# Kernel optimization log

Hardware: AMD Instinct MI355X
Metric: run time of the kernel (lower is better)

Reference implementation:

```python
import jax, jax.numpy as jnp
import numpy as np

TEMPERATURE = 0.8
TOP_K = 50
TOP_P = 0.9
REP_PENALTY = 1.2
FILTER_VALUE = -1e9  # stands in for -inf in HF top_k_top_p_filtering (numerically identical probs)

B, S, V = 16, 64, 50257
P = 64  # previously generated tokens per sequence


def setup_inputs() -> dict:
    key = jax.random.key(0)
    k1, k2 = jax.random.split(key)
    logits = jax.random.normal(k1, (B, S, V), dtype=jnp.float32) * 3.0
    prev_tokens = jax.random.randint(k2, (S, P), 0, V)
    return {"logits": logits, "prev_tokens": prev_tokens}


def _repetition_penalty(logits, prev_tokens):
    # logits: [B,S,V], prev_tokens: [S,P]
    gathered = jnp.take_along_axis(logits, prev_tokens[None, :, :], axis=-1)  # [B,S,P]
    all_neg = jnp.all(gathered < 0, axis=0, keepdims=True)                    # [1,S,P]
    penalized = jnp.where(all_neg, gathered * REP_PENALTY, gathered / REP_PENALTY)
    s_idx = jnp.broadcast_to(jnp.arange(S)[:, None], prev_tokens.shape)       # [S,P]
    # scatter back (duplicate indices write identical values -> matches set() semantics)
    return logits.at[:, s_idx, prev_tokens].set(penalized)


def _top_k_top_p_filter(logits):
    # top-k: mask everything below the k-th largest logit
    if TOP_K > 0:
        kth = jax.lax.top_k(logits, TOP_K)[0][..., -1:]                       # [B,S,1]
        logits = jnp.where(logits < kth, FILTER_VALUE, logits)
    # top-p (nucleus): sort descending, mask tokens past cumulative prob TOP_P
    if TOP_P < 1.0:
        sort_idx = jnp.argsort(-logits, axis=-1)                              # [B,S,V]
        sorted_logits = jnp.take_along_axis(logits, sort_idx, axis=-1)
        cum_probs = jnp.cumsum(jax.nn.softmax(sorted_logits, axis=-1), axis=-1)
        remove_sorted = cum_probs > TOP_P
        # shift right so the first token exceeding the threshold is kept
        remove_sorted = jnp.concatenate(
            [jnp.zeros_like(remove_sorted[..., :1]), remove_sorted[..., :-1]], axis=-1)
        inv_idx = jnp.argsort(sort_idx, axis=-1)
        remove = jnp.take_along_axis(remove_sorted, inv_idx, axis=-1)
        logits = jnp.where(remove, FILTER_VALUE, logits)
    return logits


def reference(logits, prev_tokens):
    if REP_PENALTY != 1.0:
        logits = _repetition_penalty(logits, prev_tokens)
    logits = logits / TEMPERATURE
    logits = _top_k_top_p_filter(logits)
    # Categorical(logits=...) normalizes logits; return normalized log-probs
    return jax.nn.log_softmax(logits, axis=-1)
```

## Files before the change

kernel.cpp:

```cpp
#include <hip/hip_runtime.h>
#include <cstdint>
#include <cfloat>
#include <math.h>

#define BB 16
#define SS 64
#define VV 50257
#define PP 64

#define NT 512
#define NBLK 512
#define BINS 2048
#define CAP 1536
#define BMW 1572
#define KCAP 128
#define BCAP 512
#define TRAW 6.0f

typedef float f32x4 __attribute__((ext_vector_type(4)));

__device__ __forceinline__ uint32_t fkey(float f) {
    uint32_t u = __float_as_uint(f);
    return u ^ ((uint32_t)((int32_t)u >> 31) | 0x80000000u);
}
__device__ __forceinline__ float key2f(uint32_t u) {
    uint32_t b = (u & 0x80000000u) ? (u ^ 0x80000000u) : ~u;
    return __uint_as_float(b);
}

__global__ __launch_bounds__(NT)
void sch_kernel(const float* __restrict__ logits,
                const int* __restrict__ prev,
                float* __restrict__ out)
{
    const int g   = blockIdx.x;
    const int rA  = g;
    const int rB  = g + NBLK;
    const int s   = g % SS;
    const int bA  = rA / SS;
    const int bB  = rB / SS;
    const int tid = threadIdx.x;
    const float* rowA  = logits + (size_t)rA * VV;
    const float* rowB  = logits + (size_t)rB * VV;
    float*       orowA = out    + (size_t)rA * VV;
    float*       orowB = out    + (size_t)rB * VV;

    __shared__ uint32_t s_bm[BMW];
    __shared__ float    s_cv[CAP];
    __shared__ int      s_ci[CAP];
    __shared__ uint32_t s_hist[BINS];
    __shared__ uint32_t s_scan[16];
    __shared__ int      s_ptok[PP];
    __shared__ int      s_pneg[PP];
    __shared__ float    s_prawA[PP];
    __shared__ float    s_prawB[PP];
    __shared__ float    s_ppenA[PP];
    __shared__ float    s_ppenB[PP];
    __shared__ float    s_binv[BCAP];
    __shared__ double   s_v64[KCAP];
    __shared__ double   s_e64[KCAP];
    __shared__ int      s_ki[KCAP];
    __shared__ float    s_kof[KCAP];
    __shared__ int    s_cnt, s_cntinv, s_b50, s_need, s_cntb, s_k50, s_kp, s_Kk;
    __shared__ float  s_kth, s_rc;
    __shared__ double s_lse;

    for (int i = tid; i < BMW; i += NT) s_bm[i] = 0u;
    if (tid < PP) s_pneg[tid] = 1;
    if (tid == 0) { s_cnt = 0; s_cntinv = 0; }
    __syncthreads();
    for (int pair = tid; pair < PP * BB; pair += NT) {
        int ti = pair & (PP - 1);
        int b2 = pair >> 6;
        int tok = prev[s * PP + ti];
        float gg = logits[((size_t)b2 * SS + s) * (size_t)VV + tok];
        if (gg >= 0.f) atomicAnd(&s_pneg[ti], 0);
        if (b2 == 0)  s_ptok[ti]  = tok;
        if (b2 == bA) s_prawA[ti] = gg;
        if (b2 == bB) s_prawB[ti] = gg;
    }
    __syncthreads();
    if (tid < PP) {
        int neg = s_pneg[tid];
        float ga = s_prawA[tid], gb = s_prawB[tid];
        s_ppenA[tid] = neg ? (ga * 1.2f) : (ga / 1.2f);
        s_ppenB[tid] = neg ? (gb * 1.2f) : (gb / 1.2f);
        int tok = s_ptok[tid];
        atomicOr(&s_bm[tok >> 5], 1u << (tok & 31));
    }
    __syncthreads();

    auto kbit = [&](int t) -> uint32_t {
        return (s_bm[t >> 5] >> (t & 31)) & 1u;
    };
    auto addRaw = [&](int t, float raw) {
        if (raw >= TRAW) {
            int pos = atomicAdd(&s_cnt, 1);
            if (pos < CAP) { s_cv[pos] = raw; s_ci[pos] = t; }
        }
    };
    auto streamFast = [&](const float* row_) {
        const int mis   = (int)(((size_t)row_ >> 2) & 3);
        const int head  = (4 - mis) & 3;
        const int nq    = (VV - head) >> 2;
        const int ttail = head + (nq << 2);
        const float4* p4 = reinterpret_cast<const float4*>(row_ + head);
        for (int t = tid; t < head; t += NT) addRaw(t, row_[t]);
        int base = 0;
        for (; base + 4 * NT <= nq; base += 4 * NT) {
            float4 f[4];
            #pragma unroll
            for (int u = 0; u < 4; ++u) f[u] = p4[base + tid + u * NT];
            #pragma unroll
            for (int u = 0; u < 4; ++u) {
                int t = head + ((base + tid + u * NT) << 2);
                addRaw(t + 0, f[u].x);
                addRaw(t + 1, f[u].y);
                addRaw(t + 2, f[u].z);
                addRaw(t + 3, f[u].w);
            }
        }
        for (int q = base + tid; q < nq; q += NT) {
            float4 f = p4[q];
            int t = head + (q << 2);
            addRaw(t + 0, f.x); addRaw(t + 1, f.y);
            addRaw(t + 2, f.z); addRaw(t + 3, f.w);
        }
        for (int t = ttail + tid; t < VV; t += NT) addRaw(t, row_[t]);
    };
    auto procFull = [&](int t, float raw, bool doHist, float thr, const float* ppenS) {
        float v = raw;
        if (kbit(t)) {
            #pragma unroll 1
            for (int j = 0; j < PP; ++j)
                if (s_ptok[j] == t) { v = ppenS[j]; break; }
        }
        if (!doHist) {
            if (v >= thr) {
                int pos = atomicAdd(&s_cnt, 1);
                if (pos < CAP) { s_cv[pos] = v; s_ci[pos] = t; }
            }
        } else {
            atomicAdd(&s_hist[fkey(v) >> 21], 1u);
        }
    };
    auto streamFull = [&](bool doHist, float thr, const float* row_, const float* ppenS) {
        const int mis   = (int)(((size_t)row_ >> 2) & 3);
        const int head  = (4 - mis) & 3;
        const int nq    = (VV - head) >> 2;
        const int ttail = head + (nq << 2);
        const float4* p4 = reinterpret_cast<const float4*>(row_ + head);
        for (int t = tid; t < head; t += NT) procFull(t, row_[t], doHist, thr, ppenS);
        for (int q = tid; q < nq; q += NT) {
            float4 f = p4[q];
            int t = head + (q << 2);
            procFull(t + 0, f.x, doHist, thr, ppenS);
            procFull(t + 1, f.y, doHist, thr, ppenS);
            procFull(t + 2, f.z, doHist, thr, ppenS);
            procFull(t + 3, f.w, doHist, thr, ppenS);
        }
        for (int t = ttail + tid; t < VV; t += NT) procFull(t, row_[t], doHist, thr, ppenS);
    };
    auto findB50 = [&](int target) {
        __syncthreads();
        const int per = BINS / NT;
        int base = tid * per;
        uint32_t loc = 0;
        #pragma unroll
        for (int k2 = 0; k2 < per; ++k2) loc += s_hist[base + k2];
        uint32_t incl = loc;
        #pragma unroll
        for (int off = 1; off < 64; off <<= 1) {
            uint32_t u = (uint32_t)__shfl_up((int)incl, off, 64);
            if ((tid & 63) >= off) incl += u;
        }
        int wid = tid >> 6;
        if ((tid & 63) == 63) s_scan[wid] = incl;
        __syncthreads();
        if (tid < 8) {
            uint32_t p = 0;
            for (int w = 0; w < tid; ++w) p += s_scan[w];
            s_scan[8 + tid] = p;
        }
        __syncthreads();
        uint32_t pre_incl = s_scan[8 + wid] + incl;
        uint32_t total    = s_scan[8 + 7] + s_scan[7];
        uint32_t run = total - pre_incl;
        for (int k2 = per - 1; k2 >= 0; --k2) {
            uint32_t h = s_hist[base + k2];
            uint32_t run2 = run + h;
            if (run < (uint32_t)target && run2 >= (uint32_t)target) {
                s_b50 = base + k2;
                s_need = target - (int)run;
            }
            run = run2;
        }
        __syncthreads();
    };
    auto doFallback = [&](const float* row_, const float* ppenS) {
        for (int i = tid; i < BINS; i += NT) s_hist[i] = 0u;
        __syncthreads();
        streamFull(true, 0.f, row_, ppenS);
        findB50(50);
        float thrF = key2f((uint32_t)s_b50 << 21);
        if (tid == 0) s_cnt = 0;
        __syncthreads();
        streamFull(false, thrF, row_, ppenS);
        __syncthreads();
    };
    auto computeKth = [&]() {
        for (int i = tid; i < BINS; i += NT) s_hist[i] = 0u;
        if (tid == 0) { s_cntb = 0; s_kth = -FLT_MAX; }
        __syncthreads();
        int cc = min(s_cnt, CAP);
        for (int i = tid; i < cc; i += NT)
            atomicAdd(&s_hist[fkey(s_cv[i]) >> 21], 1u);
        findB50(50);
        int b50 = s_b50, need = s_need;
        for (int i = tid; i < cc; i += NT) {
            if ((int)(fkey(s_cv[i]) >> 21) == b50) {
                int p = atomicAdd(&s_cntb, 1);
                if (p < BCAP) s_binv[p] = s_cv[i];
            }
        }
        __syncthreads();
        int cb = min(s_cntb, BCAP);
        for (int i = tid; i < cb; i += NT) {
            float vi = s_binv[i];
            int gt = 0, ge = 0;
            for (int j = 0; j < cb; ++j) {
                float vj = s_binv[j];
                gt += (vj > vi);
                ge += (vj >= vi);
            }
            if (gt < need && ge >= need) s_kth = vi;
        }
        __syncthreads();
    };

    auto midPhases = [&](const float* row_, const float* prawS, const float* ppenS) {
        const int cntRaw = min(s_cnt, CAP);
        for (int i = tid; i < cntRaw; i += NT) {
            if (kbit(s_ci[i])) {
                s_cv[i] = -FLT_MAX;
                atomicAdd(&s_cntinv, 1);
            }
        }
        __syncthreads();
        if (tid < PP) {
            int tok = s_ptok[tid];
            bool first = true;
            for (int j = 0; j < tid; ++j)
                if (s_ptok[j] == tok) { first = false; break; }
            if (first) {
                int pos = atomicAdd(&s_cnt, 1);
                if (pos < CAP) { s_cv[pos] = ppenS[tid]; s_ci[pos] = tok; }
            }
        }
        __syncthreads();
        bool fellback = false;
        {
            bool okc = (s_cnt <= CAP) && ((cntRaw - s_cntinv) >= 50);
            if (!okc) { doFallback(row_, ppenS); fellback = true; }
        }
        computeKth();
        if (!fellback && (s_kth - 1e-4f < TRAW)) {
            doFallback(row_, ppenS);
            computeKth();
        }
        if (tid == 0) s_k50 = 0;
        __syncthreads();
        const float gthr = s_kth - 1e-4f;
        const int cntc = min(s_cnt, CAP);
        for (int i = tid; i < cntc; i += NT) {
            if (s_cv[i] >= gthr) {
                int p = atomicAdd(&s_k50, 1);
                if (p < KCAP) {
                    int tok = s_ci[i];
                    double v64;
                    if (kbit(tok)) {
                        int pj = 0;
                        #pragma unroll 1
                        for (int j = 0; j < PP; ++j)
                            if (s_ptok[j] == tok) { pj = j; break; }
                        double gd = (double)prawS[pj];
                        double pen = s_pneg[pj] ? (gd * 1.2) : (gd / 1.2);
                        v64 = pen / 0.8;
                    } else {
                        v64 = (double)s_cv[i] / 0.8;
                    }
                    s_v64[p] = v64;
                    s_ki[p]  = tok;
                }
            }
        }
        __syncthreads();
        const int k50c = min(s_k50, KCAP);
        for (int i = k50c + tid; i < KCAP; i += NT) {
            s_v64[i] = -1e300;
            s_ki[i]  = (1 << 30) + i;
        }
        __syncthreads();
        if (tid < 64) {
            int l = tid;
            double v0 = s_v64[l],    v1 = s_v64[l + 64];
            int    i0 = s_ki[l],     i1 = s_ki[l + 64];
            for (int k = 2; k <= KCAP; k <<= 1) {
                for (int j = k >> 1; j > 0; j >>= 1) {
                    if (j >= 64) {
                        bool before = (v0 > v1) || (v0 == v1 && i0 < i1);
                        if (!before) {
                            double tv = v0; v0 = v1; v1 = tv;
                            int    ti = i0; i0 = i1; i1 = ti;
                        }
                    } else {
                        double nv0 = __shfl_xor(v0, j, 64);
                        double nv1 = __shfl_xor(v1, j, 64);
                        int    ni0 = __shfl_xor(i0, j, 64);
                        int    ni1 = __shfl_xor(i1, j, 64);
                        bool lower = ((l & j) == 0);
                        bool up0 = ((l & k) == 0);
                        bool up1 = (((l + 64) & k) == 0);
                        bool bm0 = (v0 > nv0) || (v0 == nv0 && i0 < ni0);
                        bool bm1 = (v1 > nv1) || (v1 == nv1 && i1 < ni1);
                        bool keep0 = lower ? (up0 == bm0) : (up0 != bm0);
                        bool keep1 = lower ? (up1 == bm1) : (up1 != bm1);
                        if (!keep0) { v0 = nv0; i0 = ni0; }
                        if (!keep1) { v1 = nv1; i1 = ni1; }
                    }
                }
            }
            s_v64[l] = v0; s_v64[l + 64] = v1;
            s_ki[l]  = i0; s_ki[l + 64]  = i1;
        }
        __syncthreads();
        if (tid == 0) {
            int kk = k50c;
            int Kkept;
            if (kk <= 50) Kkept = kk;
            else {
                double kth64 = s_v64[49];
                Kkept = 50;
                while (Kkept < kk && s_v64[Kkept] == kth64) ++Kkept;
            }
            s_Kk = Kkept;
        }
        __syncthreads();
        const int Kk = s_Kk;
        const double mx = s_v64[0];
        if (tid < Kk) s_e64[tid] = exp(s_v64[tid] - mx);
        __syncthreads();
        if (tid == 0) {
            double D = 0.0;
            #pragma unroll 1
            for (int i = 0; i < Kk; ++i) D += s_e64[i];
            double c = 0.0;
            int Kp = 0;
            #pragma unroll 1
            for (int i = 0; i < Kk; ++i) {
                bool keep = (i == 0) || (c <= 0.9);
                c += s_e64[i] / D;
                if (keep) Kp = i + 1; else break;
            }
            double D2 = 0.0;
            #pragma unroll 1
            for (int i = 0; i < Kp; ++i) D2 += s_e64[i];
            double lse = log(D2);
            s_lse = lse;
            s_rc = (float)((-1e9 - mx) - lse);
            s_kp = Kp;
        }
        __syncthreads();
        if (tid < s_kp) s_kof[tid] = (float)((s_v64[tid] - mx) - s_lse);
        __syncthreads();
    };

    streamFast(rowA);
    __syncthreads();
    midPhases(rowA, s_prawA, s_ppenA);
    const int   kpA = s_kp;
    const float rcA = s_rc;
    if (tid == 0) { s_cnt = 0; s_cntinv = 0; }
    __syncthreads();

    {
        const int omis   = (int)(((size_t)orowA >> 2) & 3);
        const int ohead  = (4 - omis) & 3;
        const int onq    = (VV - ohead) >> 2;
        const int ottail = ohead + (onq << 2);
        f32x4* o4 = reinterpret_cast<f32x4*>(orowA + ohead);
        f32x4 rc4; rc4.x = rcA; rc4.y = rcA; rc4.z = rcA; rc4.w = rcA;

        const int mis   = (int)(((size_t)rowB >> 2) & 3);
        const int head  = (4 - mis) & 3;
        const int nq    = (VV - head) >> 2;
        const int ttail = head + (nq << 2);
        const float4* p4 = reinterpret_cast<const float4*>(rowB + head);

        for (int t = tid; t < ohead; t += NT)
            __builtin_nontemporal_store(rcA, &orowA[t]);
        for (int t = tid; t < head; t += NT) addRaw(t, rowB[t]);

        const int common = min(onq, nq);
        int base = 0;
        for (; base + 2 * NT <= common; base += 2 * NT) {
            float4 f0 = p4[base + tid];
            float4 f1 = p4[base + tid + NT];
            __builtin_nontemporal_store(rc4, &o4[base + tid]);
            __builtin_nontemporal_store(rc4, &o4[base + tid + NT]);
            int t0 = head + ((base + tid) << 2);
            int t1 = head + ((base + tid + NT) << 2);
            addRaw(t0 + 0, f0.x); addRaw(t0 + 1, f0.y);
            addRaw(t0 + 2, f0.z); addRaw(t0 + 3, f0.w);
            addRaw(t1 + 0, f1.x); addRaw(t1 + 1, f1.y);
            addRaw(t1 + 2, f1.z); addRaw(t1 + 3, f1.w);
        }
        for (int q = base + tid; q < common; q += NT) {
            float4 f = p4[q];
            __builtin_nontemporal_store(rc4, &o4[q]);
            int t = head + (q << 2);
            addRaw(t + 0, f.x); addRaw(t + 1, f.y);
            addRaw(t + 2, f.z); addRaw(t + 3, f.w);
        }
        for (int q = common + tid; q < onq; q += NT)
            __builtin_nontemporal_store(rc4, &o4[q]);
        for (int q = common + tid; q < nq; q += NT) {
            float4 f = p4[q];
            int t = head + (q << 2);
            addRaw(t + 0, f.x); addRaw(t + 1, f.y);
            addRaw(t + 2, f.z); addRaw(t + 3, f.w);
        }
        for (int t = ottail + tid; t < VV; t += NT)
            __builtin_nontemporal_store(rcA, &orowA[t]);
        for (int t = ttail + tid; t < VV; t += NT) addRaw(t, rowB[t]);
    }
    __syncthreads();
    if (tid < kpA) orowA[s_ki[tid]] = s_kof[tid];

    midPhases(rowB, s_prawB, s_ppenB);
    {
        const float rcB = s_rc;
        const int omis   = (int)(((size_t)orowB >> 2) & 3);
        const int ohead  = (4 - omis) & 3;
        const int onq    = (VV - ohead) >> 2;
        const int ottail = ohead + (onq << 2);
        f32x4* o4 = reinterpret_cast<f32x4*>(orowB + ohead);
        f32x4 rc4; rc4.x = rcB; rc4.y = rcB; rc4.z = rcB; rc4.w = rcB;
        for (int t = tid; t < ohead; t += NT)
            __builtin_nontemporal_store(rcB, &orowB[t]);
        for (int q = tid; q < onq; q += NT)
            __builtin_nontemporal_store(rc4, &o4[q]);
        for (int t = ottail + tid; t < VV; t += NT)
            __builtin_nontemporal_store(rcB, &orowB[t]);
    }
    __syncthreads();
    if (tid < s_kp) orowB[s_ki[tid]] = s_kof[tid];
}

extern "C" void kernel_launch(void* const* d_in, const int* in_sizes, int n_in,
                              void* d_out, int out_size, void* d_ws, size_t ws_size,
                              hipStream_t stream) {
    const float* logits = (const float*)d_in[0];
    const int*   prev   = (const int*)d_in[1];
    float*       out    = (float*)d_out;
    dim3 grid(NBLK), block(NT);
    hipLaunchKernelGGL(sch_kernel, grid, block, 0, stream, logits, prev, out);
}
```

Before: 107.7 us.

## Warp-specialize block: half runs selection phases while other half streams rows

Result: faster. 89.99 us (-16.4%).

```diff
diff --git a/kernel.cpp b/kernel.cpp
--- a/kernel.cpp
+++ b/kernel.cpp
@@ -8,7 +8,8 @@
 #define VV 50257
 #define PP 64
 
-#define NT 512
+#define NT 1024
+#define HNT 512
 #define NBLK 512
 #define BINS 2048
 #define CAP 1536
@@ -48,6 +49,8 @@
     __shared__ uint32_t s_bm[BMW];
     __shared__ float    s_cv[CAP];
     __shared__ int      s_ci[CAP];
+    __shared__ float    s_cv2[CAP];
+    __shared__ int      s_ci2[CAP];
     __shared__ uint32_t s_hist[BINS];
     __shared__ uint32_t s_scan[16];
     __shared__ int      s_ptok[PP];
@@ -61,13 +64,16 @@
     __shared__ double   s_e64[KCAP];
     __shared__ int      s_ki[KCAP];
     __shared__ float    s_kof[KCAP];
-    __shared__ int    s_cnt, s_cntinv, s_b50, s_need, s_cntb, s_k50, s_kp, s_Kk;
+    __shared__ int      s_kiA[KCAP];
+    __shared__ float    s_kofA[KCAP];
+    __shared__ int    s_cnt, s_cnt2, s_cntinv, s_b50, s_need, s_cntb, s_k50, s_kp, s_Kk;
+    __shared__ int    s_hbar;
     __shared__ float  s_kth, s_rc;
     __shared__ double s_lse;
 
     for (int i = tid; i < BMW; i += NT) s_bm[i] = 0u;
     if (tid < PP) s_pneg[tid] = 1;
-    if (tid == 0) { s_cnt = 0; s_cntinv = 0; }
+    if (tid == 0) { s_cnt = 0; s_cnt2 = 0; s_cntinv = 0; s_hbar = 0; }
     __syncthreads();
     for (int pair = tid; pair < PP * BB; pair += NT) {
         int ti = pair & (PP - 1);
@@ -90,45 +96,74 @@
     }
     __syncthreads();
 
+    int hb_phase = 0;
+    auto halfbar = [&]() {
+        __threadfence_block();
+        if ((tid & 63) == 0) atomicAdd(&s_hbar, 1);
+        ++hb_phase;
+        while (*(volatile int*)&s_hbar < 8 * hb_phase)
+            __builtin_amdgcn_s_sleep(1);
+        __threadfence_block();
+    };
+
     auto kbit = [&](int t) -> uint32_t {
         return (s_bm[t >> 5] >> (t & 31)) & 1u;
     };
-    auto addRaw = [&](int t, float raw) {
+    auto addRawP = [&](int t, float raw, float* cv, int* ci, int* pcnt) {
         if (raw >= TRAW) {
-            int pos = atomicAdd(&s_cnt, 1);
-            if (pos < CAP) { s_cv[pos] = raw; s_ci[pos] = t; }
-        }
-    };
-    auto streamFast = [&](const float* row_) {
+            int pos = atomicAdd(pcnt, 1);
+            if (pos < CAP) { cv[pos] = raw; ci[pos] = t; }
+        }
+    };
+    auto streamFastP = [&](const float* row_, float* cv, int* ci, int* pcnt,
+                           int t0, int nthr) {
         const int mis   = (int)(((size_t)row_ >> 2) & 3);
         const int head  = (4 - mis) & 3;
         const int nq    = (VV - head) >> 2;
         const int ttail = head + (nq << 2);
         const float4* p4 = reinterpret_cast<const float4*>(row_ + head);
-        for (int t = tid; t < head; t += NT) addRaw(t, row_[t]);
+        for (int t = t0; t < head; t += nthr) addRawP(t, row_[t], cv, ci, pcnt);
         int base = 0;
-        for (; base + 4 * NT <= nq; base += 4 * NT) {
+        for (; base + 4 * nthr <= nq; base += 4 * nthr) {
             float4 f[4];
             #pragma unroll
-            for (int u = 0; u < 4; ++u) f[u] = p4[base + tid + u * NT];
+            for (int u = 0; u < 4; ++u) f[u] = p4[base + t0 + u * nthr];
             #pragma unroll
             for (int u = 0; u < 4; ++u) {
-                int t = head + ((base + tid + u * NT) << 2);
-                addRaw(t + 0, f[u].x);
-                addRaw(t + 1, f[u].y);
-                addRaw(t + 2, f[u].z);
-                addRaw(t + 3, f[u].w);
-            }
-        }
-        for (int q = base + tid; q < nq; q += NT) {
+                int t = head + ((base + t0 + u * nthr) << 2);
+                addRawP(t + 0, f[u].x, cv, ci, pcnt);
+                addRawP(t + 1, f[u].y, cv, ci, pcnt);
+                addRawP(t + 2, f[u].z, cv, ci, pcnt);
+                addRawP(t + 3, f[u].w, cv, ci, pcnt);
+            }
+        }
+        for (int q = base + t0; q < nq; q += nthr) {
             float4 f = p4[q];
             int t = head + (q << 2);
-            addRaw(t + 0, f.x); addRaw(t + 1, f.y);
-            addRaw(t + 2, f.z); addRaw(t + 3, f.w);
-        }
-        for (int t = ttail + tid; t < VV; t += NT) addRaw(t, row_[t]);
-    };
-    auto procFull = [&](int t, float raw, bool doHist, float thr, const float* ppenS) {
+            addRawP(t + 0, f.x, cv, ci, pcnt);
+            addRawP(t + 1, f.y, cv, ci, pcnt);
+            addRawP(t + 2, f.z, cv, ci, pcnt);
+            addRawP(t + 3, f.w, cv, ci, pcnt);
+        }
+        for (int t = ttail + t0; t < VV; t += nthr) addRawP(t, row_[t], cv, ci, pcnt);
+    };
+    auto ntFill = [&](float* orow_, float rc_, int t0, int nthr) {
+        const int omis   = (int)(((size_t)orow_ >> 2) & 3);
+        const int ohead  = (4 - omis) & 3;
+        const int onq    = (VV - ohead) >> 2;
+        const int ottail = ohead + (onq << 2);
+        f32x4* o4 = reinterpret_cast<f32x4*>(orow_ + ohead);
+        f32x4 rc4; rc4.x = rc_; rc4.y = rc_; rc4.z = rc_; rc4.w = rc_;
+        for (int t = t0; t < ohead; t += nthr)
+            __builtin_nontemporal_store(rc_, &orow_[t]);
+        for (int q = t0; q < onq; q += nthr)
+            __builtin_nontemporal_store(rc4, &o4[q]);
+        for (int t = ottail + t0; t < VV; t += nthr)
+            __builtin_nontemporal_store(rc_, &orow_[t]);
+    };
+
+    auto procFullH = [&](int t, float raw, bool doHist, float thr, const float* ppenS,
+                         float* cv, int* ci, int* pcnt) {
         float v = raw;
         if (kbit(t)) {
             #pragma unroll 1
@@ -137,33 +172,34 @@
         }
         if (!doHist) {
             if (v >= thr) {
-                int pos = atomicAdd(&s_cnt, 1);
-                if (pos < CAP) { s_cv[pos] = v; s_ci[pos] = t; }
+                int pos = atomicAdd(pcnt, 1);
+                if (pos < CAP) { cv[pos] = v; ci[pos] = t; }
             }
         } else {
             atomicAdd(&s_hist[fkey(v) >> 21], 1u);
         }
     };
-    auto streamFull = [&](bool doHist, float thr, const float* row_, const float* ppenS) {
+    auto streamFullH = [&](bool doHist, float thr, const float* row_, const float* ppenS,
+                           float* cv, int* ci, int* pcnt) {
         const int mis   = (int)(((size_t)row_ >> 2) & 3);
         const int head  = (4 - mis) & 3;
         const int nq    = (VV - head) >> 2;
         const int ttail = head + (nq << 2);
         const float4* p4 = reinterpret_cast<const float4*>(row_ + head);
-        for (int t = tid; t < head; t += NT) procFull(t, row_[t], doHist, thr, ppenS);
-        for (int q = tid; q < nq; q += NT) {
+        for (int t = tid; t < head; t += HNT) procFullH(t, row_[t], doHist, thr, ppenS, cv, ci, pcnt);
+        for (int q = tid; q < nq; q += HNT) {
             float4 f = p4[q];
             int t = head + (q << 2);
-            procFull(t + 0, f.x, doHist, thr, ppenS);
-            procFull(t + 1, f.y, doHist, thr, ppenS);
-            procFull(t + 2, f.z, doHist, thr, ppenS);
-            procFull(t + 3, f.w, doHist, thr, ppenS);
-        }
-        for (int t = ttail + tid; t < VV; t += NT) procFull(t, row_[t], doHist, thr, ppenS);
-    };
-    auto findB50 = [&](int target) {
-        __syncthreads();
-        const int per = BINS / NT;
+            procFullH(t + 0, f.x, doHist, thr, ppenS, cv, ci, pcnt);
+            procFullH(t + 1, f.y, doHist, thr, ppenS, cv, ci, pcnt);
+            procFullH(t + 2, f.z, doHist, thr, ppenS, cv, ci, pcnt);
+            procFullH(t + 3, f.w, doHist, thr, ppenS, cv, ci, pcnt);
+        }
+        for (int t = ttail + tid; t < VV; t += HNT) procFullH(t, row_[t], doHist, thr, ppenS, cv, ci, pcnt);
+    };
+    auto findB50H = [&](int target) {
+        halfbar();
+        const int per = BINS / HNT;
         int base = tid * per;
         uint32_t loc = 0;
         #pragma unroll
@@ -176,13 +212,13 @@
         }
         int wid = tid >> 6;
         if ((tid & 63) == 63) s_scan[wid] = incl;
-        __syncthreads();
+        halfbar();
         if (tid < 8) {
             uint32_t p = 0;
             for (int w = 0; w < tid; ++w) p += s_scan[w];
             s_scan[8 + tid] = p;
         }
-        __syncthreads();
+        halfbar();
         uint32_t pre_incl = s_scan[8 + wid] + incl;
         uint32_t total    = s_scan[8 + 7] + s_scan[7];
         uint32_t run = total - pre_incl;
@@ -195,37 +231,38 @@
             }
             run = run2;
         }
-        __syncthreads();
-    };
-    auto doFallback = [&](const float* row_, const float* ppenS) {
-        for (int i = tid; i < BINS; i += NT) s_hist[i] = 0u;
-        __syncthreads();
-        streamFull(true, 0.f, row_, ppenS);
-        findB50(50);
+        halfbar();
+    };
+    auto doFallbackH = [&](const float* row_, const float* ppenS,
+                           float* cv, int* ci, int* pcnt) {
+        for (int i = tid; i < BINS; i += HNT) s_hist[i] = 0u;
+        halfbar();
+        streamFullH(true, 0.f, row_, ppenS, cv, ci, pcnt);
+        findB50H(50);
         float thrF = key2f((uint32_t)s_b50 << 21);
-        if (tid == 0) s_cnt = 0;
-        __syncthreads();
-        streamFull(false, thrF, row_, ppenS);
-        __syncthreads();
-    };
-    auto computeKth = [&]() {
-        for (int i = tid; i < BINS; i += NT) s_hist[i] = 0u;
+        if (tid == 0) *pcnt = 0;
+        halfbar();
+        streamFullH(false, thrF, row_, ppenS, cv, ci, pcnt);
+        halfbar();
+    };
+    auto computeKthH = [&](float* cv, int* pcnt) {
+        for (int i = tid; i < BINS; i += HNT) s_hist[i] = 0u;
         if (tid == 0) { s_cntb = 0; s_kth = -FLT_MAX; }
-        __syncthreads();
-        int cc = min(s_cnt, CAP);
-        for (int i = tid; i < cc; i += NT)
-            atomicAdd(&s_hist[fkey(s_cv[i]) >> 21], 1u);
-        findB50(50);
+        halfbar();
+        int cc = min(*pcnt, CAP);
+        for (int i = tid; i < cc; i += HNT)
+            atomicAdd(&s_hist[fkey(cv[i]) >> 21], 1u);
+        findB50H(50);
         int b50 = s_b50, need = s_need;
-        for (int i = tid; i < cc; i += NT) {
-            if ((int)(fkey(s_cv[i]) >> 21) == b50) {
+        for (int i = tid; i < cc; i += HNT) {
+            if ((int)(fkey(cv[i]) >> 21) == b50) {
                 int p = atomicAdd(&s_cntb, 1);
-                if (p < BCAP) s_binv[p] = s_cv[i];
-            }
-        }
-        __syncthreads();
+                if (p < BCAP) s_binv[p] = cv[i];
+            }
+        }
+        halfbar();
         int cb = min(s_cntb, BCAP);
-        for (int i = tid; i < cb; i += NT) {
+        for (int i = tid; i < cb; i += HNT) {
             float vi = s_binv[i];
             int gt = 0, ge = 0;
             for (int j = 0; j < cb; ++j) {
@@ -235,48 +272,48 @@
             }
             if (gt < need && ge >= need) s_kth = vi;
         }
-        __syncthreads();
-    };
-
-    auto midPhases = [&](const float* row_, const float* prawS, const float* ppenS) {
-        const int cntRaw = min(s_cnt, CAP);
-        for (int i = tid; i < cntRaw; i += NT) {
-            if (kbit(s_ci[i])) {
-                s_cv[i] = -FLT_MAX;
+        halfbar();
+    };
+    auto midPhasesH = [&](const float* row_, const float* prawS, const float* ppenS,
+                          float* cv, int* ci, int* pcnt) {
+        const int cntRaw = min(*pcnt, CAP);
+        for (int i = tid; i < cntRaw; i += HNT) {
+            if (kbit(ci[i])) {
+                cv[i] = -FLT_MAX;
                 atomicAdd(&s_cntinv, 1);
             }
         }
-        __syncthreads();
+        halfbar();
         if (tid < PP) {
             int tok = s_ptok[tid];
             bool first = true;
             for (int j = 0; j < tid; ++j)
                 if (s_ptok[j] == tok) { first = false; break; }
             if (first) {
-                int pos = atomicAdd(&s_cnt, 1);
-                if (pos < CAP) { s_cv[pos] = ppenS[tid]; s_ci[pos] = tok; }
-            }
-        }
-        __syncthreads();
+                int pos = atomicAdd(pcnt, 1);
+                if (pos < CAP) { cv[pos] = ppenS[tid]; ci[pos] = tok; }
+            }
+        }
+        halfbar();
         bool fellback = false;
         {
-            bool okc = (s_cnt <= CAP) && ((cntRaw - s_cntinv) >= 50);
-            if (!okc) { doFallback(row_, ppenS); fellback = true; }
-        }
-        computeKth();
+            bool okc = (*pcnt <= CAP) && ((cntRaw - s_cntinv) >= 50);
+            if (!okc) { doFallbackH(row_, ppenS, cv, ci, pcnt); fellback = true; }
+        }
+        computeKthH(cv, pcnt);
         if (!fellback && (s_kth - 1e-4f < TRAW)) {
-            doFallback(row_, ppenS);
-            computeKth();
+            doFallbackH(row_, ppenS, cv, ci, pcnt);
+            computeKthH(cv, pcnt);
         }
         if (tid == 0) s_k50 = 0;
-        __syncthreads();
+        halfbar();
         const float gthr = s_kth - 1e-4f;
-        const int cntc = min(s_cnt, CAP);
-        for (int i = tid; i < cntc; i += NT) {
-            if (s_cv[i] >= gthr) {
+        const int cntc = min(*pcnt, CAP);
+        for (int i = tid; i < cntc; i += HNT) {
+            if (cv[i] >= gthr) {
                 int p = atomicAdd(&s_k50, 1);
                 if (p < KCAP) {
-                    int tok = s_ci[i];
+                    int tok = ci[i];
                     double v64;
                     if (kbit(tok)) {
                         int pj = 0;
@@ -287,20 +324,20 @@
                         double pen = s_pneg[pj] ? (gd * 1.2) : (gd / 1.2);
                         v64 = pen / 0.8;
                     } else {
-                        v64 = (double)s_cv[i] / 0.8;
+                        v64 = (double)cv[i] / 0.8;
                     }
                     s_v64[p] = v64;
                     s_ki[p]  = tok;
                 }
             }
         }
-        __syncthreads();
+        halfbar();
         const int k50c = min(s_k50, KCAP);
-        for (int i = k50c + tid; i < KCAP; i += NT) {
+        for (int i = k50c + tid; i < KCAP; i += HNT) {
             s_v64[i] = -1e300;
             s_ki[i]  = (1 << 30) + i;
         }
-        __syncthreads();
+        halfbar();
         if (tid < 64) {
             int l = tid;
             double v0 = s_v64[l],    v1 = s_v64[l + 64];
@@ -333,7 +370,7 @@
             s_v64[l] = v0; s_v64[l + 64] = v1;
             s_ki[l]  = i0; s_ki[l + 64]  = i1;
         }
-        __syncthreads();
+        halfbar();
         if (tid == 0) {
             int kk = k50c;
             int Kkept;
@@ -345,11 +382,11 @@
             }
             s_Kk = Kkept;
         }
-        __syncthreads();
+        halfbar();
         const int Kk = s_Kk;
         const double mx = s_v64[0];
         if (tid < Kk) s_e64[tid] = exp(s_v64[tid] - mx);
-        __syncthreads();
+        halfbar();
         if (tid == 0) {
             double D = 0.0;
             #pragma unroll 1
@@ -370,89 +407,37 @@
             s_rc = (float)((-1e9 - mx) - lse);
             s_kp = Kp;
         }
-        __syncthreads();
+        halfbar();
         if (tid < s_kp) s_kof[tid] = (float)((s_v64[tid] - mx) - s_lse);
-        __syncthreads();
-    };
-
-    streamFast(rowA);
-    __syncthreads();
-    midPhases(rowA, s_prawA, s_ppenA);
+        halfbar();
+    };
+
+    streamFastP(rowA, s_cv, s_ci, &s_cnt, tid, NT);
+    __syncthreads();
+
+    if (tid < HNT) {
+        midPhasesH(rowA, s_prawA, s_ppenA, s_cv, s_ci, &s_cnt);
+    } else {
+        streamFastP(rowB, s_cv2, s_ci2, &s_cnt2, tid - HNT, HNT);
+    }
+    __syncthreads();
+
+    const float rcA = s_rc;
     const int   kpA = s_kp;
-    const float rcA = s_rc;
-    if (tid == 0) { s_cnt = 0; s_cntinv = 0; }
-    __syncthreads();
-
-    {
-        const int omis   = (int)(((size_t)orowA >> 2) & 3);
-        const int ohead  = (4 - omis) & 3;
-        const int onq    = (VV - ohead) >> 2;
-        const int ottail = ohead + (onq << 2);
-        f32x4* o4 = reinterpret_cast<f32x4*>(orowA + ohead);
-        f32x4 rc4; rc4.x = rcA; rc4.y = rcA; rc4.z = rcA; rc4.w = rcA;
-
-        const int mis   = (int)(((size_t)rowB >> 2) & 3);
-        const int head  = (4 - mis) & 3;
-        const int nq    = (VV - head) >> 2;
-        const int ttail = head + (nq << 2);
-        const float4* p4 = reinterpret_cast<const float4*>(rowB + head);
-
-        for (int t = tid; t < ohead; t += NT)
-            __builtin_nontemporal_store(rcA, &orowA[t]);
-        for (int t = tid; t < head; t += NT) addRaw(t, rowB[t]);
-
-        const int common = min(onq, nq);
-        int base = 0;
-        for (; base + 2 * NT <= common; base += 2 * NT) {
-            float4 f0 = p4[base + tid];
-            float4 f1 = p4[base + tid + NT];
-            __builtin_nontemporal_store(rc4, &o4[base + tid]);
-            __builtin_nontemporal_store(rc4, &o4[base + tid + NT]);
-            int t0 = head + ((base + tid) << 2);
-            int t1 = head + ((base + tid + NT) << 2);
-            addRaw(t0 + 0, f0.x); addRaw(t0 + 1, f0.y);
-            addRaw(t0 + 2, f0.z); addRaw(t0 + 3, f0.w);
-            addRaw(t1 + 0, f1.x); addRaw(t1 + 1, f1.y);
-            addRaw(t1 + 2, f1.z); addRaw(t1 + 3, f1.w);
-        }
-        for (int q = base + tid; q < common; q += NT) {
-            float4 f = p4[q];
-            __builtin_nontemporal_store(rc4, &o4[q]);
-            int t = head + (q << 2);
-            addRaw(t + 0, f.x); addRaw(t + 1, f.y);
-            addRaw(t + 2, f.z); addRaw(t + 3, f.w);
-        }
-        for (int q = common + tid; q < onq; q += NT)
-            __builtin_nontemporal_store(rc4, &o4[q]);
-        for (int q = common + tid; q < nq; q += NT) {
-            float4 f = p4[q];
-            int t = head + (q << 2);
-            addRaw(t + 0, f.x); addRaw(t + 1, f.y);
-            addRaw(t + 2, f.z); addRaw(t + 3, f.w);
-        }
-        for (int t = ottail + tid; t < VV; t += NT)
-            __builtin_nontemporal_store(rcA, &orowA[t]);
-        for (int t = ttail + tid; t < VV; t += NT) addRaw(t, rowB[t]);
+    if (tid < KCAP) { s_kiA[tid] = s_ki[tid]; s_kofA[tid] = s_kof[tid]; }
+    if (tid == 0) s_cntinv = 0;
+    __syncthreads();
+
+    if (tid < HNT) {
+        midPhasesH(rowB, s_prawB, s_ppenB, s_cv2, s_ci2, &s_cnt2);
+    } else {
+        ntFill(orowA, rcA, tid - HNT, HNT);
     }
     __syncthreads();
-    if (tid < kpA) orowA[s_ki[tid]] = s_kof[tid];
-
-    midPhases(rowB, s_prawB, s_ppenB);
-    {
-        const float rcB = s_rc;
-        const int omis   = (int)(((size_t)orowB >> 2) & 3);
-        const int ohead  = (4 - omis) & 3;
-        const int onq    = (VV - ohead) >> 2;
-        const int ottail = ohead + (onq << 2);
-        f32x4* o4 = reinterpret_cast<f32x4*>(orowB + ohead);
-        f32x4 rc4; rc4.x = rcB; rc4.y = rcB; rc4.z = rcB; rc4.w = rcB;
-        for (int t = tid; t < ohead; t += NT)
-            __builtin_nontemporal_store(rcB, &orowB[t]);
-        for (int q = tid; q < onq; q += NT)
-            __builtin_nontemporal_store(rc4, &o4[q]);
-        for (int t = ottail + tid; t < VV; t += NT)
-            __builtin_nontemporal_store(rcB, &orowB[t]);
-    }
+
+    if (tid < kpA) orowA[s_kiA[tid]] = s_kofA[tid];
+    const float rcB = s_rc;
+    ntFill(orowB, rcB, tid, NT);
     __syncthreads();
     if (tid < s_kp) orowB[s_ki[tid]] = s_kof[tid];
 }
```

## Split output writing into separate producer/consumer blocks synchronized via workspace flags

Applied to the files above, without the earlier changes.

Result: slower. 173.7 us (+61.3%).

```diff
diff --git a/kernel.cpp b/kernel.cpp
--- a/kernel.cpp
+++ b/kernel.cpp
@@ -9,13 +9,16 @@
 #define PP 64
 
 #define NT 512
-#define NBLK 512
+#define NBLKC 512
+#define GRID 1024
 #define BINS 2048
 #define CAP 1536
 #define BMW 1572
 #define KCAP 128
 #define BCAP 512
 #define TRAW 6.0f
+#define MAGIC 0x5AC0FFEEu
+
 
 typedef float f32x4 __attribute__((ext_vector_type(4)));
 
@@ -31,19 +34,64 @@
 __global__ __launch_bounds__(NT)
 void sch_kernel(const float* __restrict__ logits,
                 const int* __restrict__ prev,
-                float* __restrict__ out)
+                float* __restrict__ out,
+                unsigned int* __restrict__ ws)
 {
+    unsigned int* wflag = ws;
+    unsigned int* wrc   = ws + 1024;
+    unsigned int* wkp   = ws + 2048;
+    unsigned int* wki   = ws + 3072;
+    unsigned int* wkof  = ws + 3072 + 1024 * 64;
+
+    const int tid = threadIdx.x;
+
+    if (blockIdx.x >= NBLKC) {
+        const int f = blockIdx.x - NBLKC;
+        #pragma unroll 1
+        for (int half = 0; half < 2; ++half) {
+            const int rr = f + half * NBLKC;
+            float* orow = out + (size_t)rr * VV;
+            if (tid == 0) {
+                while (atomicAdd(&wflag[rr], 0u) != MAGIC)
+                    __builtin_amdgcn_s_sleep(8);
+                __threadfence();
+            }
+            __syncthreads();
+            const int   kp = (int)atomicAdd(&wkp[rr], 0u);
+            const float rc = __uint_as_float(atomicAdd(&wrc[rr], 0u));
+            int ki_t = 0; float ko_t = 0.f;
+            if (tid < kp) {
+                ki_t = (int)atomicAdd(&wki[rr * 64 + tid], 0u);
+                ko_t = __uint_as_float(atomicAdd(&wkof[rr * 64 + tid], 0u));
+            }
+            const int omis   = (int)(((size_t)orow >> 2) & 3);
+            const int ohead  = (4 - omis) & 3;
+            const int onq    = (VV - ohead) >> 2;
+            const int ottail = ohead + (onq << 2);
+            f32x4* o4 = reinterpret_cast<f32x4*>(orow + ohead);
+            f32x4 rc4; rc4.x = rc; rc4.y = rc; rc4.z = rc; rc4.w = rc;
+            for (int t = tid; t < ohead; t += NT)
+                __builtin_nontemporal_store(rc, &orow[t]);
+            for (int q = tid; q < onq; q += NT)
+                __builtin_nontemporal_store(rc4, &o4[q]);
+            for (int t = ottail + tid; t < VV; t += NT)
+                __builtin_nontemporal_store(rc, &orow[t]);
+            __syncthreads();
+            if (tid < kp) orow[ki_t] = ko_t;
+            if (tid == 0) atomicExch(&wflag[rr], 0u);
+            __syncthreads();
+        }
+        return;
+    }
+
     const int g   = blockIdx.x;
     const int rA  = g;
-    const int rB  = g + NBLK;
+    const int rB  = g + NBLKC;
     const int s   = g % SS;
     const int bA  = rA / SS;
     const int bB  = rB / SS;
-    const int tid = threadIdx.x;
-    const float* rowA  = logits + (size_t)rA * VV;
-    const float* rowB  = logits + (size_t)rB * VV;
-    float*       orowA = out    + (size_t)rA * VV;
-    float*       orowB = out    + (size_t)rB * VV;
+    const float* rowA = logits + (size_t)rA * VV;
+    const float* rowB = logits + (size_t)rB * VV;
 
     __shared__ uint32_t s_bm[BMW];
     __shared__ float    s_cv[CAP];
@@ -237,7 +285,6 @@
         }
         __syncthreads();
     };
-
     auto midPhases = [&](const float* row_, const float* prawS, const float* ppenS) {
         const int cntRaw = min(s_cnt, CAP);
         for (int i = tid; i < cntRaw; i += NT) {
@@ -374,87 +421,32 @@
         if (tid < s_kp) s_kof[tid] = (float)((s_v64[tid] - mx) - s_lse);
         __syncthreads();
     };
+    auto publish = [&](int r) {
+        if (tid < s_kp) {
+            wki[r * 64 + tid]  = (unsigned int)s_ki[tid];
+            wkof[r * 64 + tid] = __float_as_uint(s_kof[tid]);
+        }
+        if (tid == 0) {
+            wrc[r] = __float_as_uint(s_rc);
+            wkp[r] = (unsigned int)s_kp;
+        }
+        __syncthreads();
+        if (tid == 0) {
+            __threadfence();
+            atomicExch(&wflag[r], MAGIC);
+        }
+    };
 
     streamFast(rowA);
     __syncthreads();
     midPhases(rowA, s_prawA, s_ppenA);
-    const int   kpA = s_kp;
-    const float rcA = s_rc;
+    publish(rA);
     if (tid == 0) { s_cnt = 0; s_cntinv = 0; }
     __syncthreads();
-
-    {
-        const int omis   = (int)(((size_t)orowA >> 2) & 3);
-        const int ohead  = (4 - omis) & 3;
-        const int onq    = (VV - ohead) >> 2;
-        const int ottail = ohead + (onq << 2);
-        f32x4* o4 = reinterpret_cast<f32x4*>(orowA + ohead);
-        f32x4 rc4; rc4.x = rcA; rc4.y = rcA; rc4.z = rcA; rc4.w = rcA;
-
-        const int mis   = (int)(((size_t)rowB >> 2) & 3);
-        const int head  = (4 - mis) & 3;
-        const int nq    = (VV - head) >> 2;
-        const int ttail = head + (nq << 2);
-        const float4* p4 = reinterpret_cast<const float4*>(rowB + head);
-
-        for (int t = tid; t < ohead; t += NT)
-            __builtin_nontemporal_store(rcA, &orowA[t]);
-        for (int t = tid; t < head; t += NT) addRaw(t, rowB[t]);
-
-        const int common = min(onq, nq);
-        int base = 0;
-        for (; base + 2 * NT <= common; base += 2 * NT) {
-            float4 f0 = p4[base + tid];
-            float4 f1 = p4[base + tid + NT];
-            __builtin_nontemporal_store(rc4, &o4[base + tid]);
-            __builtin_nontemporal_store(rc4, &o4[base + tid + NT]);
-            int t0 = head + ((base + tid) << 2);
-            int t1 = head + ((base + tid + NT) << 2);
-            addRaw(t0 + 0, f0.x); addRaw(t0 + 1, f0.y);
-            addRaw(t0 + 2, f0.z); addRaw(t0 + 3, f0.w);
-            addRaw(t1 + 0, f1.x); addRaw(t1 + 1, f1.y);
-            addRaw(t1 + 2, f1.z); addRaw(t1 + 3, f1.w);
-        }
-        for (int q = base + tid; q < common; q += NT) {
-            float4 f = p4[q];
-            __builtin_nontemporal_store(rc4, &o4[q]);
-            int t = head + (q << 2);
-            addRaw(t + 0, f.x); addRaw(t + 1, f.y);
-            addRaw(t + 2, f.z); addRaw(t + 3, f.w);
-        }
-        for (int q = common + tid; q < onq; q += NT)
-            __builtin_nontemporal_store(rc4, &o4[q]);
-        for (int q = common + tid; q < nq; q += NT) {
-            float4 f = p4[q];
-            int t = head + (q << 2);
-            addRaw(t + 0, f.x); addRaw(t + 1, f.y);
-            addRaw(t + 2, f.z); addRaw(t + 3, f.w);
-        }
-        for (int t = ottail + tid; t < VV; t += NT)
-            __builtin_nontemporal_store(rcA, &orowA[t]);
-        for (int t = ttail + tid; t < VV; t += NT) addRaw(t, rowB[t]);
-    }
-    __syncthreads();
-    if (tid < kpA) orowA[s_ki[tid]] = s_kof[tid];
-
+    streamFast(rowB);
+    __syncthreads();
     midPhases(rowB, s_prawB, s_ppenB);
-    {
-        const float rcB = s_rc;
-        const int omis   = (int)(((size_t)orowB >> 2) & 3);
-        const int ohead  = (4 - omis) & 3;
-        const int onq    = (VV - ohead) >> 2;
-        const int ottail = ohead + (onq << 2);
-        f32x4* o4 = reinterpret_cast<f32x4*>(orowB + ohead);
-        f32x4 rc4; rc4.x = rcB; rc4.y = rcB; rc4.z = rcB; rc4.w = rcB;
-        for (int t = tid; t < ohead; t += NT)
-            __builtin_nontemporal_store(rcB, &orowB[t]);
-        for (int q = tid; q < onq; q += NT)
-            __builtin_nontemporal_store(rc4, &o4[q]);
-        for (int t = ottail + tid; t < VV; t += NT)
-            __builtin_nontemporal_store(rcB, &orowB[t]);
-    }
-    __syncthreads();
-    if (tid < s_kp) orowB[s_ki[tid]] = s_kof[tid];
+    publish(rB);
 }
 
 extern "C" void kernel_launch(void* const* d_in, const int* in_sizes, int n_in,
@@ -463,6 +455,7 @@
     const float* logits = (const float*)d_in[0];
     const int*   prev   = (const int*)d_in[1];
     float*       out    = (float*)d_out;
-    dim3 grid(NBLK), block(NT);
-    hipLaunchKernelGGL(sch_kernel, grid, block, 0, stream, logits, prev, out);
+    unsigned int* ws    = (unsigned int*)d_ws;
+    dim3 grid(GRID), block(NT);
+    hipLaunchKernelGGL(sch_kernel, grid, block, 0, stream, logits, prev, out, ws);
 }
```
